# Optimization experiments

Hardware: AMD Instinct MI355X
Metric: run time of the kernel (lower is better)

The kernel has to match this reference:

```python
import jax, jax.numpy as jnp
import numpy as np

N = 10000
D_IN = 256
D_OUT = 128


def setup_inputs() -> dict:
    key = jax.random.key(0)
    ks = jax.random.split(key, 8)
    H_k = jax.random.normal(ks[0], (N, D_IN), dtype=jnp.float32)
    A = (jax.random.uniform(ks[1], (N, N)) < 0.003).astype(jnp.float32)
    W_w = jax.random.normal(ks[2], (D_OUT, D_IN), dtype=jnp.float32) * (1.0 / np.sqrt(D_IN))
    W_b = jax.random.normal(ks[3], (D_OUT,), dtype=jnp.float32) * 0.01
    vkt_w = jax.random.normal(ks[4], (1, D_OUT), dtype=jnp.float32) * (1.0 / np.sqrt(D_OUT))
    vkt_b = jax.random.normal(ks[5], (1,), dtype=jnp.float32) * 0.01
    vkr_w = jax.random.normal(ks[6], (1, D_OUT), dtype=jnp.float32) * (1.0 / np.sqrt(D_OUT))
    vkr_b = jax.random.normal(ks[7], (1,), dtype=jnp.float32) * 0.01
    return {"H_k": H_k, "A": A, "W_w": W_w, "W_b": W_b,
            "vkt_w": vkt_w, "vkt_b": vkt_b, "vkr_w": vkr_w, "vkr_b": vkr_b}


def reference(H_k, A, W_w, W_b, vkt_w, vkt_b, vkr_w, vkr_b):
    WH = jax.nn.relu(H_k @ W_w.T + W_b)            # [N, D_OUT]
    s = WH @ vkt_w.T + vkt_b                        # [N, 1] sender scores
    r = WH @ vkr_w.T + vkr_b                        # [N, 1] receiver scores
    # M_s[i,j] = A[i,j] * s[j] ; M_r = (A * r.T).T  => M_r[i,j] = A[j,i] * r[i]
    M = A * s.reshape(1, N) + A.T * r.reshape(N, 1)  # [N, N]
    # torch F.softmax with no dim on a 2D tensor -> softmax over dim=1
    Attention = jax.nn.softmax(jax.nn.sigmoid(M), axis=1)
    return Attention @ WH                            # [N, D_OUT]
```

## Files before the change

### kernel.cpp

```cpp
#include <hip/hip_runtime.h>
#include <math.h>

#define N 10000
#define DIN 256
#define DOUT 128
#define CAP 192
#define C0 1.6487212707001282f

__global__ __launch_bounds__(256) void k_gemm(
        const float* __restrict__ H, const float* __restrict__ W,
        const float* __restrict__ Wb,
        const float* __restrict__ vt, const float* __restrict__ vtb,
        const float* __restrict__ vr, const float* __restrict__ vrb,
        float* __restrict__ WH, float* __restrict__ s_out, float* __restrict__ r_out,
        int* __restrict__ rowcount, float* __restrict__ colsum)
{
    __shared__ float hs[32 * 260];
    __shared__ float wt[64 * 132];
    const int t = threadIdx.x;
    const int brow = blockIdx.x * 32;

    {
        if (t < 32) {
            int idx = blockIdx.x * 32 + t;
            if (idx < N) rowcount[idx] = 0;
        }
        if (blockIdx.x == 0 && t < DOUT) colsum[t] = 0.f;
    }

    #pragma unroll
    for (int l = 0; l < 8; ++l) {
        int fid = t + l * 256;
        int row = fid >> 6;
        int f4  = fid & 63;
        int grow = brow + row;
        float4 v = make_float4(0.f, 0.f, 0.f, 0.f);
        if (grow < N) v = *(const float4*)(H + (size_t)grow * DIN + f4 * 4);
        *(float4*)(hs + row * 260 + f4 * 4) = v;
    }

    float acc[4][4];
    #pragma unroll
    for (int i = 0; i < 4; ++i)
        #pragma unroll
        for (int j = 0; j < 4; ++j) acc[i][j] = 0.f;

    const int tx = t & 31;
    const int ty = t >> 5;

    for (int kc = 0; kc < 4; ++kc) {
        __syncthreads();
        #pragma unroll
        for (int l = 0; l < 8; ++l) {
            int fid = t + l * 256;
            int col = fid >> 4;
            int kq  = fid & 15;
            float4 v = *(const float4*)(W + (size_t)col * DIN + kc * 64 + kq * 4);
            wt[(kq * 4 + 0) * 132 + col] = v.x;
            wt[(kq * 4 + 1) * 132 + col] = v.y;
            wt[(kq * 4 + 2) * 132 + col] = v.z;
            wt[(kq * 4 + 3) * 132 + col] = v.w;
        }
        __syncthreads();
        #pragma unroll 4
        for (int k = 0; k < 64; ++k) {
            float4 w4 = *(const float4*)(wt + k * 132 + tx * 4);
            int gk = kc * 64 + k;
            float h0 = hs[(ty * 4 + 0) * 260 + gk];
            float h1 = hs[(ty * 4 + 1) * 260 + gk];
            float h2 = hs[(ty * 4 + 2) * 260 + gk];
            float h3 = hs[(ty * 4 + 3) * 260 + gk];
            acc[0][0] += h0 * w4.x; acc[0][1] += h0 * w4.y; acc[0][2] += h0 * w4.z; acc[0][3] += h0 * w4.w;
            acc[1][0] += h1 * w4.x; acc[1][1] += h1 * w4.y; acc[1][2] += h1 * w4.z; acc[1][3] += h1 * w4.w;
            acc[2][0] += h2 * w4.x; acc[2][1] += h2 * w4.y; acc[2][2] += h2 * w4.z; acc[2][3] += h2 * w4.w;
            acc[3][0] += h3 * w4.x; acc[3][1] += h3 * w4.y; acc[3][2] += h3 * w4.z; acc[3][3] += h3 * w4.w;
        }
    }

    __syncthreads();
    float4 bias = *(const float4*)(Wb + tx * 4);
    #pragma unroll
    for (int i = 0; i < 4; ++i) {
        int row = ty * 4 + i;
        int grow = brow + row;
        float4 o;
        o.x = fmaxf(acc[i][0] + bias.x, 0.f);
        o.y = fmaxf(acc[i][1] + bias.y, 0.f);
        o.z = fmaxf(acc[i][2] + bias.z, 0.f);
        o.w = fmaxf(acc[i][3] + bias.w, 0.f);
        *(float4*)(wt + row * 132 + tx * 4) = o;
        if (grow < N) *(float4*)(WH + (size_t)grow * DOUT + tx * 4) = o;
    }
    __syncthreads();

    const int wv = t >> 6, ln = t & 63;
    float vt0 = vt[2 * ln], vt1 = vt[2 * ln + 1];
    float vr0 = vr[2 * ln], vr1 = vr[2 * ln + 1];
    for (int rr = 0; rr < 8; ++rr) {
        int row = wv * 8 + rr;
        float a = wt[row * 132 + 2 * ln];
        float b = wt[row * 132 + 2 * ln + 1];
        float sp = a * vt0 + b * vt1;
        float rp = a * vr0 + b * vr1;
        #pragma unroll
        for (int off = 32; off; off >>= 1) {
            sp += __shfl_xor(sp, off);
            rp += __shfl_xor(rp, off);
        }
        int grow = brow + row;
        if (ln == 0 && grow < N) {
            s_out[grow] = sp + vtb[0];
            r_out[grow] = rp + vrb[0];
        }
    }
}

__global__ __launch_bounds__(256) void k_scan(const float* __restrict__ A,
        const float* __restrict__ WH,
        int* __restrict__ rowcount, unsigned* __restrict__ rowdata,
        float* __restrict__ colsum)
{
    if (blockIdx.x < 79) {
        int col = threadIdx.x & 127;
        int rbase = blockIdx.x * 128 + (threadIdx.x >> 7);
        float cs = 0.f;
        #pragma unroll 4
        for (int k = 0; k < 64; ++k) {
            int row = rbase + 2 * k;
            if (row < N) cs += WH[(size_t)row * DOUT + col];
        }
        atomicAdd(&colsum[col], cs);
    }

    const uint4* Au = (const uint4*)A;
    const size_t stride = (size_t)gridDim.x * blockDim.x;
    const size_t total4 = (size_t)N * (size_t)N / 4;
    size_t i = (size_t)blockIdx.x * blockDim.x + threadIdx.x;

#define EMIT(E) do { \
        unsigned p_ = (E) / (unsigned)N; \
        unsigned q_ = (E) - p_ * (unsigned)N; \
        int pos_ = atomicAdd(&rowcount[p_], 1); \
        if (pos_ < CAP) rowdata[(size_t)p_ * CAP + pos_] = q_; \
        int pos2_ = atomicAdd(&rowcount[q_], 1); \
        if (pos2_ < CAP) rowdata[(size_t)q_ * CAP + pos2_] = p_ | 0x8000u; \
    } while (0)

#define SCAN_BODY(I) do { \
        uint4 v_ = Au[I]; \
        if (v_.x | v_.y | v_.z | v_.w) { \
            unsigned eb_ = (unsigned)((I) * 4); \
            if (v_.x) EMIT(eb_); \
            if (v_.y) EMIT(eb_ + 1); \
            if (v_.z) EMIT(eb_ + 2); \
            if (v_.w) EMIT(eb_ + 3); \
        } } while (0)

    for (; i + stride < total4; i += 2 * stride) {
        SCAN_BODY(i);
        SCAN_BODY(i + stride);
    }
    for (; i < total4; i += stride) SCAN_BODY(i);
#undef SCAN_BODY
#undef EMIT
}

__global__ __launch_bounds__(256) void k_out(const float* __restrict__ WH,
        const float* __restrict__ s, const float* __restrict__ r,
        const float* __restrict__ colsum, const int* __restrict__ rowcount,
        const unsigned* __restrict__ rowdata, float* __restrict__ out)
{
    __shared__ unsigned ent[4][CAP];
    __shared__ float del[4][CAP];
    const int wv = threadIdx.x >> 6, ln = threadIdx.x & 63;
    const int row = blockIdx.x * 4 + wv;
    int n = rowcount[row]; if (n > CAP) n = CAP;
    const float rrow = r[row];

    unsigned my[3]; int myslot[3]; int nslots = 0;
    for (int slot = ln; slot < n; slot += 64) {
        unsigned e = rowdata[(size_t)row * CAP + slot];
        ent[wv][slot] = e;
        my[nslots] = e; myslot[nslots] = slot; nslots++;
    }
    __syncthreads();

    bool addr_[3] = {false, false, false}, dead[3] = {false, false, false};
    for (int j = 0; j < n; ++j) {
        unsigned bc = ent[wv][j];
        #pragma unroll
        for (int k = 0; k < 3; ++k) {
            if (k < nslots && myslot[k] != j) {
                unsigned mine = my[k];
                if (((mine ^ bc) & 0x8000u) && ((mine & 0x3FFFu) == (bc & 0x3FFFu))) {
                    if (mine & 0x8000u) dead[k] = true;
                    else addr_[k] = true;
                }
            }
        }
    }

    float zpart = 0.f;
    #pragma unroll
    for (int k = 0; k < 3; ++k) {
        if (k < nslots) {
            float dlt = 0.f;
            if (!dead[k]) {
                unsigned col = my[k] & 0x3FFFu;
                float m = (my[k] & 0x8000u) ? rrow : s[col];
                if (addr_[k]) m += rrow;
                float sg = 1.f / (1.f + __expf(-m));
                dlt = expf(sg) - C0;
            }
            del[wv][myslot[k]] = dlt;
            zpart += dlt;
        }
    }
    #pragma unroll
    for (int off = 32; off; off >>= 1) zpart += __shfl_xor(zpart, off);
    __syncthreads();

    float acc0 = 0.f, acc1 = 0.f;
    for (int e2 = 0; e2 < n; ++e2) {
        float dlt = del[wv][e2];
        if (dlt != 0.f) {
            unsigned col = ent[wv][e2] & 0x3FFFu;
            float2 w2 = *(const float2*)(WH + (size_t)col * DOUT + 2 * ln);
            acc0 += dlt * w2.x;
            acc1 += dlt * w2.y;
        }
    }
    float inv = 1.f / (C0 * (float)N + zpart);
    int d = 2 * ln;
    out[(size_t)row * DOUT + d]     = (C0 * colsum[d]     + acc0) * inv;
    out[(size_t)row * DOUT + d + 1] = (C0 * colsum[d + 1] + acc1) * inv;
}

extern "C" void kernel_launch(void* const* d_in, const int* in_sizes, int n_in,
                              void* d_out, int out_size, void* d_ws, size_t ws_size,
                              hipStream_t stream)
{
    (void)in_sizes; (void)n_in; (void)out_size; (void)ws_size;
    const float* H   = (const float*)d_in[0];
    const float* A   = (const float*)d_in[1];
    const float* W   = (const float*)d_in[2];
    const float* Wb  = (const float*)d_in[3];
    const float* vt  = (const float*)d_in[4];
    const float* vtb = (const float*)d_in[5];
    const float* vr  = (const float*)d_in[6];
    const float* vrb = (const float*)d_in[7];

    char* ws = (char*)d_ws;
    size_t off = 0;
    float* WH = (float*)(ws + off);        off += (size_t)N * DOUT * 4;
    float* s_ = (float*)(ws + off);        off += 40960;
    float* r_ = (float*)(ws + off);        off += 40960;
    float* colsum = (float*)(ws + off);    off += 1024;
    int* rowcount = (int*)(ws + off);      off += 40960;
    unsigned* rowdata = (unsigned*)(ws + off);

    k_gemm<<<(N + 31) / 32, 256, 0, stream>>>(H, W, Wb, vt, vtb, vr, vrb,
                                              WH, s_, r_, rowcount, colsum);
    k_scan<<<2048, 256, 0, stream>>>(A, WH, rowcount, rowdata, colsum);
    k_out<<<N / 4, 256, 0, stream>>>(WH, s_, r_, colsum, rowcount, rowdata, (float*)d_out);
}
```

Measured before the change: 291.1 us.

## Decouple dense adjacency scan from per-row bucket building via staged pair list

The scan kernel no longer does two global atomics per nonzero while streaming A. It appends each nonzero index to a block-local shared buffer and flushes that buffer to a global pair list with one atomic per block. A new kernel then builds the per-row CSR buckets from the compact list. This keeps the 400MB streaming scan close to bandwidth-bound, at the cost of an extra launch, an intermediate buffer, and a hard cap on the total number of pairs.

Measured after the change: 300.4 us. 3.2% more time.

```diff
diff --git a/kernel.cpp b/kernel.cpp
--- a/kernel.cpp
+++ b/kernel.cpp
@@ -5,6 +5,8 @@
 #define DIN 256
 #define DOUT 128
 #define CAP 192
+#define MAXP 400000
+#define LBUF 2048
 #define C0 1.6487212707001282f
 
 __global__ __launch_bounds__(256) void k_gemm(
@@ -13,7 +15,7 @@
         const float* __restrict__ vt, const float* __restrict__ vtb,
         const float* __restrict__ vr, const float* __restrict__ vrb,
         float* __restrict__ WH, float* __restrict__ s_out, float* __restrict__ r_out,
-        int* __restrict__ rowcount, float* __restrict__ colsum)
+        int* __restrict__ rowcount, float* __restrict__ colsum, int* __restrict__ gcnt)
 {
     __shared__ float hs[32 * 260];
     __shared__ float wt[64 * 132];
@@ -25,7 +27,10 @@
             int idx = blockIdx.x * 32 + t;
             if (idx < N) rowcount[idx] = 0;
         }
-        if (blockIdx.x == 0 && t < DOUT) colsum[t] = 0.f;
+        if (blockIdx.x == 0) {
+            if (t < DOUT) colsum[t] = 0.f;
+            if (t == 255) gcnt[0] = 0;
+        }
     }
 
     #pragma unroll
@@ -117,9 +122,15 @@
 
 __global__ __launch_bounds__(256) void k_scan(const float* __restrict__ A,
         const float* __restrict__ WH,
-        int* __restrict__ rowcount, unsigned* __restrict__ rowdata,
+        unsigned* __restrict__ pairs, int* __restrict__ gcnt,
         float* __restrict__ colsum)
 {
+    __shared__ unsigned pbuf[LBUF];
+    __shared__ int pcnt;
+    __shared__ int gbase;
+    if (threadIdx.x == 0) pcnt = 0;
+    __syncthreads();
+
     if (blockIdx.x < 79) {
         int col = threadIdx.x & 127;
         int rbase = blockIdx.x * 128 + (threadIdx.x >> 7);
@@ -137,23 +148,20 @@
     const size_t total4 = (size_t)N * (size_t)N / 4;
     size_t i = (size_t)blockIdx.x * blockDim.x + threadIdx.x;
 
-#define EMIT(E) do { \
-        unsigned p_ = (E) / (unsigned)N; \
-        unsigned q_ = (E) - p_ * (unsigned)N; \
-        int pos_ = atomicAdd(&rowcount[p_], 1); \
-        if (pos_ < CAP) rowdata[(size_t)p_ * CAP + pos_] = q_; \
-        int pos2_ = atomicAdd(&rowcount[q_], 1); \
-        if (pos2_ < CAP) rowdata[(size_t)q_ * CAP + pos2_] = p_ | 0x8000u; \
+#define PUSH(E) do { \
+        int pos_ = atomicAdd(&pcnt, 1); \
+        if (pos_ < LBUF) pbuf[pos_] = (E); \
+        else { int gp_ = atomicAdd(gcnt, 1); if (gp_ < MAXP) pairs[gp_] = (E); } \
     } while (0)
 
 #define SCAN_BODY(I) do { \
         uint4 v_ = Au[I]; \
         if (v_.x | v_.y | v_.z | v_.w) { \
             unsigned eb_ = (unsigned)((I) * 4); \
-            if (v_.x) EMIT(eb_); \
-            if (v_.y) EMIT(eb_ + 1); \
-            if (v_.z) EMIT(eb_ + 2); \
-            if (v_.w) EMIT(eb_ + 3); \
+            if (v_.x) PUSH(eb_); \
+            if (v_.y) PUSH(eb_ + 1); \
+            if (v_.z) PUSH(eb_ + 2); \
+            if (v_.w) PUSH(eb_ + 3); \
         } } while (0)
 
     for (; i + stride < total4; i += 2 * stride) {
@@ -162,7 +170,35 @@
     }
     for (; i < total4; i += stride) SCAN_BODY(i);
 #undef SCAN_BODY
-#undef EMIT
+#undef PUSH
+
+    __syncthreads();
+    int cnt = pcnt; if (cnt > LBUF) cnt = LBUF;
+    if (threadIdx.x == 0 && cnt > 0) gbase = atomicAdd(gcnt, cnt);
+    __syncthreads();
+    if (cnt > 0) {
+        int base = gbase;
+        for (int k = threadIdx.x; k < cnt; k += 256) {
+            int gp = base + k;
+            if (gp < MAXP) pairs[gp] = pbuf[k];
+        }
+    }
+}
+
+__global__ __launch_bounds__(256) void k_build(const unsigned* __restrict__ pairs,
+        const int* __restrict__ gcnt, int* __restrict__ rowcount,
+        unsigned* __restrict__ rowdata)
+{
+    int npair = gcnt[0]; if (npair > MAXP) npair = MAXP;
+    int tid = blockIdx.x * 256 + threadIdx.x;
+    if (tid >= npair) return;
+    unsigned e = pairs[tid];
+    unsigned p = e / (unsigned)N;
+    unsigned q = e - p * (unsigned)N;
+    int pos = atomicAdd(&rowcount[p], 1);
+    if (pos < CAP) rowdata[(size_t)p * CAP + pos] = q;
+    int pos2 = atomicAdd(&rowcount[q], 1);
+    if (pos2 < CAP) rowdata[(size_t)q * CAP + pos2] = p | 0x8000u;
 }
 
 __global__ __launch_bounds__(256) void k_out(const float* __restrict__ WH,
@@ -257,10 +293,13 @@
     float* r_ = (float*)(ws + off);        off += 40960;
     float* colsum = (float*)(ws + off);    off += 1024;
     int* rowcount = (int*)(ws + off);      off += 40960;
+    int* gcnt = (int*)(ws + off);          off += 256;
+    unsigned* pairs = (unsigned*)(ws + off); off += (size_t)MAXP * 4;
     unsigned* rowdata = (unsigned*)(ws + off);
 
     k_gemm<<<(N + 31) / 32, 256, 0, stream>>>(H, W, Wb, vt, vtb, vr, vrb,
-                                              WH, s_, r_, rowcount, colsum);
-    k_scan<<<2048, 256, 0, stream>>>(A, WH, rowcount, rowdata, colsum);
+                                              WH, s_, r_, rowcount, colsum, gcnt);
+    k_scan<<<2048, 256, 0, stream>>>(A, WH, pairs, gcnt, colsum);
+    k_build<<<(MAXP + 255) / 256, 256, 0, stream>>>(pairs, gcnt, rowcount, rowdata);
     k_out<<<N / 4, 256, 0, stream>>>(WH, s_, r_, colsum, rowcount, rowdata, (float*)d_out);
 }
```
